# Performance work log

Hardware: AMD Instinct MI355X
Metric: run time of the kernel (lower is better)

The kernel has to match this reference:

```python
import jax, jax.numpy as jnp
import numpy as np

E, H, I = 5, 768, 1024  # num_experts, hidden_dim, intermediate_dim
TOP_K = 2


def setup_inputs() -> dict:
    key = jax.random.key(0)
    ks = jax.random.split(key, 6)
    s = 0.02
    return {
        "x": jax.random.normal(ks[0], (4, 2048, H), dtype=jnp.float32),
        "router_w": jax.random.normal(ks[1], (E, H), dtype=jnp.float32) * s,  # torch Linear (out,in)
        "router_b": jnp.zeros((E,), dtype=jnp.float32),
        "gate_w": jax.random.normal(ks[2], (E, H, I), dtype=jnp.float32) * s,
        "up_w": jax.random.normal(ks[3], (E, H, I), dtype=jnp.float32) * s,
        "down_w": jax.random.normal(ks[4], (E, I, H), dtype=jnp.float32) * s,
    }


def reference(x, router_w, router_b, gate_w, up_w, down_w):
    B, S, Hd = x.shape
    xf = x.reshape(-1, Hd)                       # [T, H]
    T = xf.shape[0]
    # Router: linear (with bias) -> softmax -> top-2 -> renormalize
    logits = xf @ router_w.T + router_b          # [T, E]
    scores = jax.nn.softmax(logits, axis=-1)
    vals, idx = jax.lax.top_k(scores, TOP_K)     # [T, 2]
    vals = vals / jnp.sum(vals, axis=-1, keepdims=True)
    # Dense combine weights: zero for unselected experts (same math as the
    # per-expert gather/scatter loop in the original module).
    comb = jnp.zeros((T, gate_w.shape[0]), dtype=x.dtype)
    comb = comb.at[jnp.arange(T)[:, None], idx].add(vals)  # [T, E]
    # SwiGLU per expert, vectorized over experts
    g = jnp.einsum('th,ehi->tei', xf, gate_w)    # [T, E, I]
    u = jnp.einsum('th,ehi->tei', xf, up_w)
    y = jnp.einsum('tei,eih->teh', jax.nn.silu(g) * u, down_w)  # [T, E, H]
    out = jnp.einsum('teh,te->th', y, comb)
    return out.reshape(B, S, Hd)
```

## Files before the change

### kernel.cpp

```cpp
#include <hip/hip_runtime.h>
#include <hip/hip_bf16.h>
#include <cstdint>
#include <cstddef>

#define T_TOK 8192
#define H_DIM 768
#define I_DIM 1024
#define N_EXP 5
#define MAXTILE 136

typedef short v8s __attribute__((ext_vector_type(8)));
typedef float v4f __attribute__((ext_vector_type(4)));

static __device__ __forceinline__ unsigned short f2bf(float f) {
    union { float f; unsigned int u; } v; v.f = f;
    unsigned int u = v.u;
    unsigned int r = (u + 0x7fffu + ((u >> 16) & 1u)) >> 16;
    return (unsigned short)r;
}
static __device__ __forceinline__ float bf2f(unsigned short s) {
    union { unsigned int u; float f; } v; v.u = ((unsigned int)s) << 16; return v.f;
}

static __device__ __forceinline__ void async16(const unsigned short* g, unsigned short* l) {
    __builtin_amdgcn_global_load_lds(
        (const __attribute__((address_space(1))) unsigned int*)g,
        (__attribute__((address_space(3))) unsigned int*)l, 16, 0, 0);
}

#define WAIT_VM4() __builtin_amdgcn_s_waitcnt(0x0F74)

__global__ void k_prep(const float* __restrict__ gw, const float* __restrict__ uw,
                       const float* __restrict__ dw,
                       unsigned short* __restrict__ wbt, unsigned short* __restrict__ dbt,
                       const float* __restrict__ x, const float* __restrict__ rw,
                       const float* __restrict__ rb, unsigned short* __restrict__ xb,
                       int* __restrict__ top2e, float2* __restrict__ top2w) {
    const int z = blockIdx.z;
    const int tid = threadIdx.x;
    if (z < 3 * N_EXP) {
        __shared__ float tile[32][33];
        const int row = tid >> 3, cq = tid & 7;
        const int ocol = tid >> 3, seg = tid & 7;
        if (z < 2 * N_EXP) {
            if (blockIdx.y >= H_DIM / 32) return;
            const int e = z % N_EXP;
            const int isUp = z >= N_EXP;
            const float* src = (isUp ? uw : gw) + (size_t)e * H_DIM * I_DIM;
            const int c0 = blockIdx.x * 32, r0 = blockIdx.y * 32;
            float4 v = *(const float4*)(src + (size_t)(r0 + row) * I_DIM + c0 + cq * 4);
            tile[row][cq * 4 + 0] = v.x; tile[row][cq * 4 + 1] = v.y;
            tile[row][cq * 4 + 2] = v.z; tile[row][cq * 4 + 3] = v.w;
            __syncthreads();
            int c = c0 + ocol;
            int orow = (c >> 4) * 32 + (c & 15) + (isUp ? 16 : 0);
            ushort4 o;
            o.x = f2bf(tile[seg * 4 + 0][ocol]); o.y = f2bf(tile[seg * 4 + 1][ocol]);
            o.z = f2bf(tile[seg * 4 + 2][ocol]); o.w = f2bf(tile[seg * 4 + 3][ocol]);
            *(ushort4*)(wbt + ((size_t)e * 2 * I_DIM + orow) * H_DIM + r0 + seg * 4) = o;
        } else {
            if (blockIdx.x >= H_DIM / 32) return;
            const int e = z - 2 * N_EXP;
            const float* src = dw + (size_t)e * I_DIM * H_DIM;
            unsigned short* dst = dbt + (size_t)e * I_DIM * H_DIM;
            const int c0 = blockIdx.x * 32, r0 = blockIdx.y * 32;
            float4 v = *(const float4*)(src + (size_t)(r0 + row) * H_DIM + c0 + cq * 4);
            tile[row][cq * 4 + 0] = v.x; tile[row][cq * 4 + 1] = v.y;
            tile[row][cq * 4 + 2] = v.z; tile[row][cq * 4 + 3] = v.w;
            __syncthreads();
            ushort4 o;
            o.x = f2bf(tile[seg * 4 + 0][ocol]); o.y = f2bf(tile[seg * 4 + 1][ocol]);
            o.z = f2bf(tile[seg * 4 + 2][ocol]); o.w = f2bf(tile[seg * 4 + 3][ocol]);
            *(ushort4*)(dst + (size_t)(c0 + ocol) * I_DIM + r0 + seg * 4) = o;
        }
    } else {
        const int wave = tid >> 6, lane = tid & 63;
        const int t = (((z - 3 * N_EXP) * 1024 + blockIdx.y * 32 + blockIdx.x) * 4) + wave;
        const float* xr = x + (size_t)t * H_DIM;
        unsigned short* xbr = xb + (size_t)t * H_DIM;
        float acc[N_EXP];
#pragma unroll
        for (int e = 0; e < N_EXP; e++) acc[e] = 0.f;
#pragma unroll
        for (int j = 0; j < H_DIM / 256; j++) {
            int idx = j * 256 + lane * 4;
            float4 xv = *(const float4*)(xr + idx);
            ushort4 o;
            o.x = f2bf(xv.x); o.y = f2bf(xv.y); o.z = f2bf(xv.z); o.w = f2bf(xv.w);
            *(ushort4*)(xbr + idx) = o;
#pragma unroll
            for (int e = 0; e < N_EXP; e++) {
                float4 wv = *(const float4*)(rw + e * H_DIM + idx);
                acc[e] += xv.x * wv.x + xv.y * wv.y + xv.z * wv.z + xv.w * wv.w;
            }
        }
#pragma unroll
        for (int s = 32; s > 0; s >>= 1) {
#pragma unroll
            for (int e = 0; e < N_EXP; e++) acc[e] += __shfl_down(acc[e], s);
        }
        if (lane == 0) {
            float l[N_EXP];
#pragma unroll
            for (int e = 0; e < N_EXP; e++) l[e] = acc[e] + rb[e];
            int i1 = 0;
#pragma unroll
            for (int e = 1; e < N_EXP; e++) if (l[e] > l[i1]) i1 = e;
            int i2 = (i1 == 0) ? 1 : 0;
#pragma unroll
            for (int e = 0; e < N_EXP; e++) if (e != i1 && l[e] > l[i2]) i2 = e;
            float w1 = 1.f / (1.f + __expf(l[i2] - l[i1]));
            top2e[t] = i1 | (i2 << 8);
            top2w[t] = make_float2(w1, 1.f - w1);
        }
    }
}

__global__ void k_router_b(const int* __restrict__ top2e, const float2* __restrict__ top2w,
                           int* __restrict__ cnt, int* __restrict__ tokslot,
                           float* __restrict__ pweight, int* __restrict__ done,
                           int4* __restrict__ tiles) {
    __shared__ int lcnt[N_EXP], lbase[N_EXP];
    const int tid = threadIdx.x;
    if (tid < N_EXP) lcnt[tid] = 0;
    __syncthreads();
    const int t = blockIdx.x * 256 + tid;
    const int pe = top2e[t];
    const float2 wv = top2w[t];
    const int e1 = pe & 0xff, e2 = pe >> 8;
    const int s1 = atomicAdd(&lcnt[e1], 1);
    const int s2 = atomicAdd(&lcnt[e2], 1);
    __syncthreads();
    if (tid < N_EXP) lbase[tid] = atomicAdd(&cnt[tid], lcnt[tid]);
    __syncthreads();
    const int p1 = lbase[e1] + s1;
    tokslot[e1 * T_TOK + p1] = t; pweight[e1 * T_TOK + p1] = wv.x;
    const int p2 = lbase[e2] + s2;
    tokslot[e2 * T_TOK + p2] = t | (1 << 16); pweight[e2 * T_TOK + p2] = wv.y;
    __syncthreads();
    if (tid == 0) {
        __threadfence();
        if (atomicAdd(done, 1) == (int)gridDim.x - 1) {
            int c[N_EXP], off = 0, idx = 0;
            for (int e = 0; e < N_EXP; e++) c[e] = atomicAdd(&cnt[e], 0);
            for (int e = 0; e < N_EXP; e++) {
                for (int m0 = 0; m0 < c[e]; m0 += 128)
                    tiles[idx++] = make_int4(e, m0, off, c[e]);
                off += c[e];
            }
            for (; idx < MAXTILE; idx++) tiles[idx] = make_int4(-1, 0, 0, 0);
        }
    }
}

__launch_bounds__(256, 3)
__global__ void k_gateup(const unsigned short* __restrict__ xb,
                         const unsigned short* __restrict__ wbt,
                         const int4* __restrict__ tiles,
                         const int* __restrict__ tokslot,
                         const float* __restrict__ pweight,
                         unsigned short* __restrict__ hbuf) {
    const int4 td = tiles[blockIdx.x];
    const int e = td.x;
    if (e < 0) return;
    const int m0 = td.y, offe = td.z, cn = td.w;
    const int n0 = blockIdx.y * 64;

    __shared__ __align__(16) unsigned short ldsA[3][128 * 32];
    __shared__ __align__(16) unsigned short ldsB[3][128 * 32];
    __shared__ int tokLds[128];
    __shared__ float pwLds[128];

    const int tid = threadIdx.x;
    if (tid < 128) {
        int gr = m0 + tid;
        int tk = 0; float pw = 0.f;
        if (gr < cn) { tk = tokslot[e * T_TOK + gr] & 0xFFFF; pw = pweight[e * T_TOK + gr]; }
        tokLds[tid] = tk; pwLds[tid] = pw;
    }
    __syncthreads();

    const int lane = tid & 63;
    const int wave = tid >> 6;
    const int fm = lane & 15, quad = lane >> 4;

    const int srow = wave * 16 + (lane >> 2);
    const int scol = (lane & 3) * 8;
    const unsigned short* aG1 = xb + (size_t)tokLds[srow] * H_DIM + scol;
    const unsigned short* aG2 = xb + (size_t)tokLds[64 + srow] * H_DIM + scol;
    const unsigned short* bG1 = wbt + ((size_t)e * 2 * I_DIM + n0 * 2 + srow) * H_DIM + scol;
    const unsigned short* bG2 = bG1 + (size_t)64 * H_DIM;
    const int ldsOff = wave * 512;

    const int wm = (wave & 1) * 64, wnw = wave >> 1;

    v4f acc[4][4];
#pragma unroll
    for (int i = 0; i < 4; i++)
#pragma unroll
        for (int j = 0; j < 4; j++) acc[i][j] = (v4f)0.f;

    const int NIT = H_DIM / 32;
    async16(aG1, &ldsA[0][ldsOff]);
    async16(aG2, &ldsA[0][2048 + ldsOff]);
    async16(bG1, &ldsB[0][ldsOff]);
    async16(bG2, &ldsB[0][2048 + ldsOff]);
    async16(aG1 + 32, &ldsA[1][ldsOff]);
    async16(aG2 + 32, &ldsA[1][2048 + ldsOff]);
    async16(bG1 + 32, &ldsB[1][ldsOff]);
    async16(bG2 + 32, &ldsB[1][2048 + ldsOff]);

    for (int kb = 0; kb < NIT; kb++) {
        const int cur = kb % 3;
        WAIT_VM4();
        __builtin_amdgcn_s_barrier();
        {
            const int kpf = (kb + 2 < NIT ? kb + 2 : NIT - 1) * 32;
            const int nb = (kb + 2) % 3;
            async16(aG1 + kpf, &ldsA[nb][ldsOff]);
            async16(aG2 + kpf, &ldsA[nb][2048 + ldsOff]);
            async16(bG1 + kpf, &ldsB[nb][ldsOff]);
            async16(bG2 + kpf, &ldsB[nb][2048 + ldsOff]);
        }
        v8s aF[4], bF[4];
#pragma unroll
        for (int im = 0; im < 4; im++)
            aF[im] = *(const v8s*)&ldsA[cur][(wm + im * 16 + fm) * 32 + quad * 8];
#pragma unroll
        for (int in = 0; in < 4; in++)
            bF[in] = *(const v8s*)&ldsB[cur][(wnw * 64 + in * 16 + fm) * 32 + quad * 8];
#pragma unroll
        for (int im = 0; im < 4; im++)
#pragma unroll
            for (int in = 0; in < 4; in++)
                acc[im][in] = __builtin_amdgcn_mfma_f32_16x16x32_bf16(aF[im], bF[in], acc[im][in], 0, 0, 0);
    }

#pragma unroll
    for (int im = 0; im < 4; im++) {
#pragma unroll
        for (int reg = 0; reg < 4; reg++) {
            int lr = wm + im * 16 + quad * 4 + reg;
            int gr = m0 + lr;
            if (gr < cn) {
                float pw = pwLds[lr];
                size_t base = (size_t)(offe + gr) * I_DIM + n0 + wnw * 32 + fm;
#pragma unroll
                for (int j = 0; j < 2; j++) {
                    float g = acc[im][2 * j][reg];
                    float u = acc[im][2 * j + 1][reg];
                    float s = g / (1.f + __expf(-g));
                    hbuf[base + j * 16] = f2bf(s * u * pw);
                }
            }
        }
    }
}

__launch_bounds__(256, 3)
__global__ void k_down(const unsigned short* __restrict__ hbuf,
                       const unsigned short* __restrict__ dbt,
                       const int4* __restrict__ tiles,
                       const int* __restrict__ tokslot,
                       unsigned short* __restrict__ ybuf) {
    const int4 td = tiles[blockIdx.x];
    const int e = td.x;
    if (e < 0) return;
    const int m0 = td.y, offe = td.z, cn = td.w;
    const int n0 = blockIdx.y * 128;

    __shared__ __align__(16) unsigned short ldsA[3][128 * 32];
    __shared__ __align__(16) unsigned short ldsB[3][128 * 32];
    __shared__ int tokLds[128];

    const int tid = threadIdx.x;
    if (tid < 128) {
        int gr = m0 + tid;
        tokLds[tid] = (gr < cn) ? tokslot[e * T_TOK + gr] : 0;
    }
    __syncthreads();

    const int lane = tid & 63;
    const int wave = tid >> 6;
    const int fm = lane & 15, quad = lane >> 4;

    const int srow = wave * 16 + (lane >> 2);
    const int scol = (lane & 3) * 8;
    int ar1 = m0 + srow;      if (ar1 >= cn) ar1 = cn - 1;
    int ar2 = m0 + 64 + srow; if (ar2 >= cn) ar2 = cn - 1;
    const unsigned short* aG1 = hbuf + (size_t)(offe + ar1) * I_DIM + scol;
    const unsigned short* aG2 = hbuf + (size_t)(offe + ar2) * I_DIM + scol;
    const unsigned short* bG1 = dbt + ((size_t)e * H_DIM + n0 + srow) * I_DIM + scol;
    const unsigned short* bG2 = bG1 + (size_t)64 * I_DIM;
    const int ldsOff = wave * 512;

    const int wm = (wave & 1) * 64, wn = (wave >> 1) * 64;

    v4f acc[4][4];
#pragma unroll
    for (int i = 0; i < 4; i++)
#pragma unroll
        for (int j = 0; j < 4; j++) acc[i][j] = (v4f)0.f;

    const int NIT = I_DIM / 32;
    async16(aG1, &ldsA[0][ldsOff]);
    async16(aG2, &ldsA[0][2048 + ldsOff]);
    async16(bG1, &ldsB[0][ldsOff]);
    async16(bG2, &ldsB[0][2048 + ldsOff]);
    async16(aG1 + 32, &ldsA[1][ldsOff]);
    async16(aG2 + 32, &ldsA[1][2048 + ldsOff]);
    async16(bG1 + 32, &ldsB[1][ldsOff]);
    async16(bG2 + 32, &ldsB[1][2048 + ldsOff]);

    for (int kb = 0; kb < NIT; kb++) {
        const int cur = kb % 3;
        WAIT_VM4();
        __builtin_amdgcn_s_barrier();
        {
            const int kpf = (kb + 2 < NIT ? kb + 2 : NIT - 1) * 32;
            const int nb = (kb + 2) % 3;
            async16(aG1 + kpf, &ldsA[nb][ldsOff]);
            async16(aG2 + kpf, &ldsA[nb][2048 + ldsOff]);
            async16(bG1 + kpf, &ldsB[nb][ldsOff]);
            async16(bG2 + kpf, &ldsB[nb][2048 + ldsOff]);
        }
        v8s aF[4], bF[4];
#pragma unroll
        for (int im = 0; im < 4; im++)
            aF[im] = *(const v8s*)&ldsA[cur][(wm + im * 16 + fm) * 32 + quad * 8];
#pragma unroll
        for (int in = 0; in < 4; in++)
            bF[in] = *(const v8s*)&ldsB[cur][(wn + in * 16 + fm) * 32 + quad * 8];
#pragma unroll
        for (int im = 0; im < 4; im++)
#pragma unroll
            for (int in = 0; in < 4; in++)
                acc[im][in] = __builtin_amdgcn_mfma_f32_16x16x32_bf16(aF[im], bF[in], acc[im][in], 0, 0, 0);
    }

#pragma unroll
    for (int im = 0; im < 4; im++) {
#pragma unroll
        for (int reg = 0; reg < 4; reg++) {
            int lr = wm + im * 16 + quad * 4 + reg;
            int gr = m0 + lr;
            if (gr < cn) {
                int v = tokLds[lr];
                int tok = v & 0xFFFF, s = (v >> 16) & 1;
#pragma unroll
                for (int in = 0; in < 4; in++) {
                    int col = n0 + wn + in * 16 + fm;
                    ybuf[((size_t)s * T_TOK + tok) * H_DIM + col] = f2bf(acc[im][in][reg]);
                }
            }
        }
    }
}

__global__ void k_combine(const unsigned short* __restrict__ ybuf, float* __restrict__ out) {
    const size_t i8 = ((size_t)blockIdx.x * 256 + threadIdx.x) * 8;
    const unsigned short* y0 = ybuf + i8;
    const unsigned short* y1 = ybuf + (size_t)T_TOK * H_DIM + i8;
    ushort4 a0 = *(const ushort4*)y0, a1 = *(const ushort4*)(y0 + 4);
    ushort4 b0 = *(const ushort4*)y1, b1 = *(const ushort4*)(y1 + 4);
    float4 o0, o1;
    o0.x = bf2f(a0.x) + bf2f(b0.x); o0.y = bf2f(a0.y) + bf2f(b0.y);
    o0.z = bf2f(a0.z) + bf2f(b0.z); o0.w = bf2f(a0.w) + bf2f(b0.w);
    o1.x = bf2f(a1.x) + bf2f(b1.x); o1.y = bf2f(a1.y) + bf2f(b1.y);
    o1.z = bf2f(a1.z) + bf2f(b1.z); o1.w = bf2f(a1.w) + bf2f(b1.w);
    *(float4*)(out + i8) = o0;
    *(float4*)(out + i8 + 4) = o1;
}

extern "C" void kernel_launch(void* const* d_in, const int* in_sizes, int n_in,
                              void* d_out, int out_size, void* d_ws, size_t ws_size,
                              hipStream_t stream) {
    const float* x  = (const float*)d_in[0];
    const float* rw = (const float*)d_in[1];
    const float* rb = (const float*)d_in[2];
    const float* gw = (const float*)d_in[3];
    const float* uw = (const float*)d_in[4];
    const float* dw = (const float*)d_in[5];
    float* out = (float*)d_out;

    char* ws = (char*)d_ws;
    size_t o = 0;
    auto alloc = [&](size_t bytes) { void* p = ws + o; o += (bytes + 255) & ~255ull; return p; };
    int*    cnt     = (int*)   alloc(8 * 4);
    int*    tokslot = (int*)   alloc((size_t)N_EXP * T_TOK * 4);
    float*  pweight = (float*) alloc((size_t)N_EXP * T_TOK * 4);
    int*    top2e   = (int*)   alloc((size_t)T_TOK * 4);
    float2* top2w   = (float2*)alloc((size_t)T_TOK * 8);
    int4*   tiles   = (int4*)  alloc((size_t)MAXTILE * 16);
    unsigned short* xb   = (unsigned short*)alloc((size_t)T_TOK * H_DIM * 2);
    unsigned short* wbt  = (unsigned short*)alloc((size_t)N_EXP * 2 * I_DIM * H_DIM * 2);
    unsigned short* dbt  = (unsigned short*)alloc((size_t)N_EXP * H_DIM * I_DIM * 2);
    unsigned short* hbuf = (unsigned short*)alloc((size_t)(2 * T_TOK + 128) * I_DIM * 2);
    unsigned short* ybuf = (unsigned short*)alloc((size_t)2 * T_TOK * H_DIM * 2);

    hipMemsetAsync(cnt, 0, 8 * 4, stream);

    dim3 pg(I_DIM / 32, I_DIM / 32, 3 * N_EXP + 2);
    k_prep<<<pg, 256, 0, stream>>>(gw, uw, dw, wbt, dbt, x, rw, rb, xb, top2e, top2w);

    k_router_b<<<T_TOK / 256, 256, 0, stream>>>(top2e, top2w, cnt, tokslot, pweight,
                                                cnt + 5, tiles);

    dim3 g1(MAXTILE, I_DIM / 64);
    k_gateup<<<g1, 256, 0, stream>>>(xb, wbt, tiles, tokslot, pweight, hbuf);

    dim3 g2(MAXTILE, H_DIM / 128);
    k_down<<<g2, 256, 0, stream>>>(hbuf, dbt, tiles, tokslot, ybuf);

    k_combine<<<(T_TOK * H_DIM) / (256 * 8), 256, 0, stream>>>(ybuf, out);
}
```

Before: 268.9 us.

## Replace triple-buffered K=32 pipeline with single-buffer K=64 XOR-swizzled LDS tiles

Result: faster. 241.1 us (-10.4%).

```diff
diff --git a/kernel.cpp b/kernel.cpp
--- a/kernel.cpp
+++ b/kernel.cpp
@@ -27,8 +27,6 @@
         (const __attribute__((address_space(1))) unsigned int*)g,
         (__attribute__((address_space(3))) unsigned int*)l, 16, 0, 0);
 }
-
-#define WAIT_VM4() __builtin_amdgcn_s_waitcnt(0x0F74)
 
 __global__ void k_prep(const float* __restrict__ gw, const float* __restrict__ uw,
                        const float* __restrict__ dw,
@@ -153,7 +151,7 @@
     }
 }
 
-__launch_bounds__(256, 3)
+__launch_bounds__(256, 4)
 __global__ void k_gateup(const unsigned short* __restrict__ xb,
                          const unsigned short* __restrict__ wbt,
                          const int4* __restrict__ tiles,
@@ -166,8 +164,8 @@
     const int m0 = td.y, offe = td.z, cn = td.w;
     const int n0 = blockIdx.y * 64;
 
-    __shared__ __align__(16) unsigned short ldsA[3][128 * 32];
-    __shared__ __align__(16) unsigned short ldsB[3][128 * 32];
+    __shared__ __align__(16) unsigned short ldsA[128 * 64];
+    __shared__ __align__(16) unsigned short ldsB[128 * 64];
     __shared__ int tokLds[128];
     __shared__ float pwLds[128];
 
@@ -184,13 +182,19 @@
     const int wave = tid >> 6;
     const int fm = lane & 15, quad = lane >> 4;
 
-    const int srow = wave * 16 + (lane >> 2);
-    const int scol = (lane & 3) * 8;
-    const unsigned short* aG1 = xb + (size_t)tokLds[srow] * H_DIM + scol;
-    const unsigned short* aG2 = xb + (size_t)tokLds[64 + srow] * H_DIM + scol;
-    const unsigned short* bG1 = wbt + ((size_t)e * 2 * I_DIM + n0 * 2 + srow) * H_DIM + scol;
-    const unsigned short* bG2 = bG1 + (size_t)64 * H_DIM;
-    const int ldsOff = wave * 512;
+    const int prow = lane >> 3;
+    const int pc = lane & 7;
+    const int lc8 = (pc ^ prow) * 8;
+
+    unsigned aOff[4];
+#pragma unroll
+    for (int c = 0; c < 4; c++)
+        aOff[c] = (unsigned)tokLds[c * 32 + wave * 8 + prow] * H_DIM;
+    const unsigned short* aBase = xb + lc8;
+    const unsigned short* bBase =
+        wbt + ((size_t)e * 2 * I_DIM + n0 * 2 + wave * 8 + prow) * H_DIM + lc8;
+    unsigned short* ldsAW = ldsA + wave * 8 * 64;
+    unsigned short* ldsBW = ldsB + wave * 8 * 64;
 
     const int wm = (wave & 1) * 64, wnw = wave >> 1;
 
@@ -200,40 +204,32 @@
 #pragma unroll
         for (int j = 0; j < 4; j++) acc[i][j] = (v4f)0.f;
 
-    const int NIT = H_DIM / 32;
-    async16(aG1, &ldsA[0][ldsOff]);
-    async16(aG2, &ldsA[0][2048 + ldsOff]);
-    async16(bG1, &ldsB[0][ldsOff]);
-    async16(bG2, &ldsB[0][2048 + ldsOff]);
-    async16(aG1 + 32, &ldsA[1][ldsOff]);
-    async16(aG2 + 32, &ldsA[1][2048 + ldsOff]);
-    async16(bG1 + 32, &ldsB[1][ldsOff]);
-    async16(bG2 + 32, &ldsB[1][2048 + ldsOff]);
-
-    for (int kb = 0; kb < NIT; kb++) {
-        const int cur = kb % 3;
-        WAIT_VM4();
-        __builtin_amdgcn_s_barrier();
-        {
-            const int kpf = (kb + 2 < NIT ? kb + 2 : NIT - 1) * 32;
-            const int nb = (kb + 2) % 3;
-            async16(aG1 + kpf, &ldsA[nb][ldsOff]);
-            async16(aG2 + kpf, &ldsA[nb][2048 + ldsOff]);
-            async16(bG1 + kpf, &ldsB[nb][ldsOff]);
-            async16(bG2 + kpf, &ldsB[nb][2048 + ldsOff]);
-        }
-        v8s aF[4], bF[4];
-#pragma unroll
-        for (int im = 0; im < 4; im++)
-            aF[im] = *(const v8s*)&ldsA[cur][(wm + im * 16 + fm) * 32 + quad * 8];
-#pragma unroll
-        for (int in = 0; in < 4; in++)
-            bF[in] = *(const v8s*)&ldsB[cur][(wnw * 64 + in * 16 + fm) * 32 + quad * 8];
-#pragma unroll
-        for (int im = 0; im < 4; im++)
+    for (int kb = 0; kb < H_DIM / 64; kb++) {
+        const int k0 = kb * 64;
+#pragma unroll
+        for (int c = 0; c < 4; c++)
+            async16(aBase + aOff[c] + k0, ldsAW + c * 32 * 64);
+#pragma unroll
+        for (int c = 0; c < 4; c++)
+            async16(bBase + (size_t)c * 32 * H_DIM + k0, ldsBW + c * 32 * 64);
+        __syncthreads();
+#pragma unroll
+        for (int ks = 0; ks < 2; ks++) {
+            const int pq = ((ks * 4 + quad) ^ (fm & 7)) * 8;
+            v8s aF[4], bF[4];
+#pragma unroll
+            for (int im = 0; im < 4; im++)
+                aF[im] = *(const v8s*)&ldsA[(wm + im * 16 + fm) * 64 + pq];
 #pragma unroll
             for (int in = 0; in < 4; in++)
-                acc[im][in] = __builtin_amdgcn_mfma_f32_16x16x32_bf16(aF[im], bF[in], acc[im][in], 0, 0, 0);
+                bF[in] = *(const v8s*)&ldsB[(wnw * 64 + in * 16 + fm) * 64 + pq];
+#pragma unroll
+            for (int im = 0; im < 4; im++)
+#pragma unroll
+                for (int in = 0; in < 4; in++)
+                    acc[im][in] = __builtin_amdgcn_mfma_f32_16x16x32_bf16(aF[im], bF[in], acc[im][in], 0, 0, 0);
+        }
+        __syncthreads();
     }
 
 #pragma unroll
@@ -257,7 +253,7 @@
     }
 }
 
-__launch_bounds__(256, 3)
+__launch_bounds__(256, 4)
 __global__ void k_down(const unsigned short* __restrict__ hbuf,
                        const unsigned short* __restrict__ dbt,
                        const int4* __restrict__ tiles,
@@ -269,8 +265,8 @@
     const int m0 = td.y, offe = td.z, cn = td.w;
     const int n0 = blockIdx.y * 128;
 
-    __shared__ __align__(16) unsigned short ldsA[3][128 * 32];
-    __shared__ __align__(16) unsigned short ldsB[3][128 * 32];
+    __shared__ __align__(16) unsigned short ldsA[128 * 64];
+    __shared__ __align__(16) unsigned short ldsB[128 * 64];
     __shared__ int tokLds[128];
 
     const int tid = threadIdx.x;
@@ -284,15 +280,22 @@
     const int wave = tid >> 6;
     const int fm = lane & 15, quad = lane >> 4;
 
-    const int srow = wave * 16 + (lane >> 2);
-    const int scol = (lane & 3) * 8;
-    int ar1 = m0 + srow;      if (ar1 >= cn) ar1 = cn - 1;
-    int ar2 = m0 + 64 + srow; if (ar2 >= cn) ar2 = cn - 1;
-    const unsigned short* aG1 = hbuf + (size_t)(offe + ar1) * I_DIM + scol;
-    const unsigned short* aG2 = hbuf + (size_t)(offe + ar2) * I_DIM + scol;
-    const unsigned short* bG1 = dbt + ((size_t)e * H_DIM + n0 + srow) * I_DIM + scol;
-    const unsigned short* bG2 = bG1 + (size_t)64 * I_DIM;
-    const int ldsOff = wave * 512;
+    const int prow = lane >> 3;
+    const int pc = lane & 7;
+    const int lc8 = (pc ^ prow) * 8;
+
+    unsigned aOff[4];
+#pragma unroll
+    for (int c = 0; c < 4; c++) {
+        int ar = m0 + c * 32 + wave * 8 + prow;
+        if (ar >= cn) ar = cn - 1;
+        aOff[c] = (unsigned)(offe + ar) * I_DIM;
+    }
+    const unsigned short* aBase = hbuf + lc8;
+    const unsigned short* bBase =
+        dbt + ((size_t)e * H_DIM + n0 + wave * 8 + prow) * I_DIM + lc8;
+    unsigned short* ldsAW = ldsA + wave * 8 * 64;
+    unsigned short* ldsBW = ldsB + wave * 8 * 64;
 
     const int wm = (wave & 1) * 64, wn = (wave >> 1) * 64;
 
@@ -302,40 +305,32 @@
 #pragma unroll
         for (int j = 0; j < 4; j++) acc[i][j] = (v4f)0.f;
 
-    const int NIT = I_DIM / 32;
-    async16(aG1, &ldsA[0][ldsOff]);
-    async16(aG2, &ldsA[0][2048 + ldsOff]);
-    async16(bG1, &ldsB[0][ldsOff]);
-    async16(bG2, &ldsB[0][2048 + ldsOff]);
-    async16(aG1 + 32, &ldsA[1][ldsOff]);
-    async16(aG2 + 32, &ldsA[1][2048 + ldsOff]);
-    async16(bG1 + 32, &ldsB[1][ldsOff]);
-    async16(bG2 + 32, &ldsB[1][2048 + ldsOff]);
-
-    for (int kb = 0; kb < NIT; kb++) {
-        const int cur = kb % 3;
-        WAIT_VM4();
-        __builtin_amdgcn_s_barrier();
-        {
-            const int kpf = (kb + 2 < NIT ? kb + 2 : NIT - 1) * 32;
-            const int nb = (kb + 2) % 3;
-            async16(aG1 + kpf, &ldsA[nb][ldsOff]);
-            async16(aG2 + kpf, &ldsA[nb][2048 + ldsOff]);
-            async16(bG1 + kpf, &ldsB[nb][ldsOff]);
-            async16(bG2 + kpf, &ldsB[nb][2048 + ldsOff]);
-        }
-        v8s aF[4], bF[4];
-#pragma unroll
-        for (int im = 0; im < 4; im++)
-            aF[im] = *(const v8s*)&ldsA[cur][(wm + im * 16 + fm) * 32 + quad * 8];
-#pragma unroll
-        for (int in = 0; in < 4; in++)
-            bF[in] = *(const v8s*)&ldsB[cur][(wn + in * 16 + fm) * 32 + quad * 8];
-#pragma unroll
-        for (int im = 0; im < 4; im++)
+    for (int kb = 0; kb < I_DIM / 64; kb++) {
+        const int k0 = kb * 64;
+#pragma unroll
+        for (int c = 0; c < 4; c++)
+            async16(aBase + aOff[c] + k0, ldsAW + c * 32 * 64);
+#pragma unroll
+        for (int c = 0; c < 4; c++)
+            async16(bBase + (size_t)c * 32 * I_DIM + k0, ldsBW + c * 32 * 64);
+        __syncthreads();
+#pragma unroll
+        for (int ks = 0; ks < 2; ks++) {
+            const int pq = ((ks * 4 + quad) ^ (fm & 7)) * 8;
+            v8s aF[4], bF[4];
+#pragma unroll
+            for (int im = 0; im < 4; im++)
+                aF[im] = *(const v8s*)&ldsA[(wm + im * 16 + fm) * 64 + pq];
 #pragma unroll
             for (int in = 0; in < 4; in++)
-                acc[im][in] = __builtin_amdgcn_mfma_f32_16x16x32_bf16(aF[im], bF[in], acc[im][in], 0, 0, 0);
+                bF[in] = *(const v8s*)&ldsB[(wn + in * 16 + fm) * 64 + pq];
+#pragma unroll
+            for (int im = 0; im < 4; im++)
+#pragma unroll
+                for (int in = 0; in < 4; in++)
+                    acc[im][in] = __builtin_amdgcn_mfma_f32_16x16x32_bf16(aF[im], bF[in], acc[im][in], 0, 0, 0);
+        }
+        __syncthreads();
     }
 
 #pragma unroll
```
